# Optimization experiments

Measured on AMD Instinct MI355X. Metric: run time of the kernel, lower is better.

## Reference

```python
import jax, jax.numpy as jnp
import numpy as np

Q = 16293   # quantization_channels
R = 24      # residual_channels
D = 32      # dilation_channels
S = 128     # skip_channels
K = 2       # filter_width
NL = 8      # number of residual blocks
B = 4       # batch_size
L = 2048    # input sequence length
RECEPTIVE = (K - 1) * sum([1, 2, 4, 8, 16, 32, 64, 128]) + K  # 257
OUT_W = L - RECEPTIVE + 1  # 1792


def setup_inputs() -> dict:
    key = jax.random.key(0)
    ks = jax.random.split(key, 9)
    sc = 0.05
    return {
        "idx": jax.random.randint(ks[0], (B, L), 0, Q, dtype=jnp.int32),
        "pre_W": jax.random.normal(ks[1], (K, Q, R), jnp.float32) * sc,
        "filt_W": jax.random.normal(ks[2], (NL, K, R, D), jnp.float32) * sc,
        "gate_W": jax.random.normal(ks[3], (NL, K, R, D), jnp.float32) * sc,
        "res_W": jax.random.normal(ks[4], (NL, D, R), jnp.float32) * sc,
        "skip_W": jax.random.normal(ks[5], (NL, D, S), jnp.float32) * sc,
        "post_W1": jax.random.normal(ks[6], (S, S), jnp.float32) * sc,
        "post_W2": jax.random.normal(ks[7], (S, Q), jnp.float32) * sc,
    }


def _conv2(x, W):
    # kernel_size=2, dilation=1 (the original passes dilations[0]=1 to every
    # block), 'valid' padding: out[t] = x[t] @ W[0] + x[t+1] @ W[1]
    return jnp.einsum('btc,cf->btf', x[:, :-1], W[0]) + \
           jnp.einsum('btc,cf->btf', x[:, 1:], W[1])


def reference(idx, pre_W, filt_W, gate_W, res_W, skip_W, post_W1, post_W2):
    # one_hot(idx, Q) followed by a width-2 conv == two-tap embedding gather
    x = pre_W[0][idx[:, :-1]] + pre_W[1][idx[:, 1:]]  # [B, L-1, R]
    skip_sum = jnp.zeros((B, OUT_W, S), x.dtype)
    for i in range(NL):
        out = jnp.tanh(_conv2(x, filt_W[i])) * jax.nn.sigmoid(_conv2(x, gate_W[i]))
        # training-mode slice: skip_cut = T_out - output_width
        out_skip = out[:, -OUT_W:]                                  # [B, OUT_W, D]
        skip_sum = skip_sum + jnp.einsum('btd,ds->bts', out_skip, skip_W[i])
        transformed = jnp.einsum('btd,dr->btr', out, res_W[i])      # [B, T-1, R]
        x = x[:, 1:] + transformed                                  # residual, cut input
    h = jax.nn.relu(skip_sum)
    h = jax.nn.relu(jnp.einsum('bts,su->btu', h, post_W1))
    logits = jnp.einsum('bts,sq->btq', h, post_W2)                  # [B, OUT_W, Q]
    return logits
```

## Files before the change

### kernel.cpp

```cpp
#include <hip/hip_runtime.h>
#include <stdint.h>

#define BB 4
#define LL 2048
#define QQ 16293
#define RR 24
#define DD 32
#define SS 128
#define NLAYER 8
#define OUTW 1792
#define TT0 2047
#define MROWS (BB*OUTW)
#define NPAD 16384
#define WCH 28

typedef float v4f __attribute__((ext_vector_type(4)));
typedef short v8s __attribute__((ext_vector_type(8)));

static __device__ __forceinline__ unsigned short f2bf(float x) {
  unsigned int u = __float_as_uint(x);
  unsigned int r = (u + 0x7fffu + ((u >> 16) & 1u)) >> 16;
  return (unsigned short)r;
}

static __device__ __forceinline__ float fast_sigmoid(float z) {
  return __builtin_amdgcn_rcpf(1.0f + __expf(-z));
}
static __device__ __forceinline__ float fast_tanh(float z) {
  return 1.0f - 2.0f * __builtin_amdgcn_rcpf(1.0f + __expf(2.0f * z));
}

__global__ __launch_bounds__(1024) void fused_layers_kernel(
    const int* __restrict__ idx, const float* __restrict__ preW,
    const float* __restrict__ filtW, const float* __restrict__ gateW,
    const float* __restrict__ resW, const float* __restrict__ skipW,
    float* __restrict__ skip_out) {
  int b = blockIdx.y;
  int j0 = blockIdx.x * WCH;
  int lane = (int)(threadIdx.x & 63);
  int w = __builtin_amdgcn_readfirstlane((int)(threadIdx.x >> 6));

  __shared__ float x_t[2][RR][66];
  __shared__ float out_s[64][33];

  for (int z = (int)threadIdx.x; z < 2 * RR * 2; z += 1024) {
    int bu = z & 1;
    int cc = 64 + ((z >> 1) & 1);
    int r = z >> 2;
    x_t[bu][r][cc] = 0.f;
  }

  int tbase = j0 + 247;
  if (w < 12) {
    int t = tbase + lane;
    if (t > TT0 - 1) t = TT0 - 1;
    int i0 = idx[b * LL + t];
    int i1 = idx[b * LL + t + 1];
    const float* p0 = preW + (size_t)i0 * RR + 2 * w;
    const float* p1 = preW + (size_t)QQ * RR + (size_t)i1 * RR + 2 * w;
#pragma unroll
    for (int rr = 0; rr < 2; ++rr)
      x_t[0][2 * w + rr][lane] = p0[rr] + p1[rr];
  }

  float sk[8];
#pragma unroll
  for (int c = 0; c < 8; ++c) sk[c] = 0.f;

  __syncthreads();

  for (int i = 0; i < NLAYER; ++i) {
    int cur = i & 1, nxt = cur ^ 1;
    int lmax = 62 - i;

    float xa[RR], xb[RR];
#pragma unroll
    for (int r = 0; r < RR; ++r) {
      xa[r] = x_t[cur][r][lane];
      xb[r] = x_t[cur][r][lane + 1];
    }
    const float* Fw = filtW + (size_t)i * 2 * RR * DD;
    const float* Gw = gateW + (size_t)i * 2 * RR * DD;
    float zf[2], zg[2];
#pragma unroll
    for (int dd = 0; dd < 2; ++dd) { zf[dd] = 0.f; zg[dd] = 0.f; }
#pragma unroll
    for (int r = 0; r < RR; ++r) {
#pragma unroll
      for (int dd = 0; dd < 2; ++dd) {
        int d = w * 2 + dd;
        zf[dd] = fmaf(xa[r], Fw[r * DD + d], zf[dd]);
        zf[dd] = fmaf(xb[r], Fw[RR * DD + r * DD + d], zf[dd]);
        zg[dd] = fmaf(xa[r], Gw[r * DD + d], zg[dd]);
        zg[dd] = fmaf(xb[r], Gw[RR * DD + r * DD + d], zg[dd]);
      }
    }
    if (lane <= lmax) {
#pragma unroll
      for (int dd = 0; dd < 2; ++dd)
        out_s[lane][w * 2 + dd] = fast_tanh(zf[dd]) * fast_sigmoid(zg[dd]);
    }
    __syncthreads();

    if (lane < WCH) {
      const float* Sw = skipW + (size_t)i * DD * SS + w * 8;
#pragma unroll
      for (int d = 0; d < DD; ++d) {
        float o = out_s[lane + 7 - i][d];
#pragma unroll
        for (int c = 0; c < 8; ++c)
          sk[c] = fmaf(o, Sw[d * SS + c], sk[c]);
      }
    }

    if (w < 12 && lane <= lmax) {
      const float* Rw = resW + (size_t)i * DD * RR;
#pragma unroll
      for (int rr = 0; rr < 2; ++rr) {
        int r = w * 2 + rr;
        float acc = x_t[cur][r][lane + 1];
#pragma unroll
        for (int d = 0; d < DD; ++d)
          acc = fmaf(out_s[lane][d], Rw[d * RR + r], acc);
        x_t[nxt][r][lane] = acc;
      }
    }
    __syncthreads();
  }

  if (lane < WCH) {
    float* sp = skip_out + ((size_t)b * OUTW + j0 + lane) * SS + w * 8;
#pragma unroll
    for (int c4 = 0; c4 < 2; ++c4) {
      float4 v;
      v.x = sk[4 * c4 + 0]; v.y = sk[4 * c4 + 1];
      v.z = sk[4 * c4 + 2]; v.w = sk[4 * c4 + 3];
      *(float4*)(sp + 4 * c4) = v;
    }
  }
}

__global__ __launch_bounds__(256) void h1_kernel(const float* __restrict__ skip_sum,
                                                 const float* __restrict__ W1,
                                                 unsigned short* __restrict__ h1) {
  int m0 = blockIdx.x * 32;
  int tc = threadIdx.x & 31;
  int tr = threadIdx.x >> 5;
  __shared__ float h_s[32][128];
#pragma unroll
  for (int it = 0; it < 16; ++it) {
    int lin = it * 256 + (int)threadIdx.x;
    int rrow = lin >> 7, d = lin & 127;
    float v = skip_sum[(size_t)(m0 + rrow) * SS + d];
    h_s[rrow][d] = v > 0.f ? v : 0.f;
  }
  __syncthreads();

  float acc[4][4];
#pragma unroll
  for (int rr = 0; rr < 4; ++rr)
#pragma unroll
    for (int c = 0; c < 4; ++c) acc[rr][c] = 0.f;

#pragma unroll 4
  for (int d = 0; d < 128; ++d) {
    float4 wv = *(const float4*)(W1 + (size_t)d * SS + tc * 4);
#pragma unroll
    for (int rr = 0; rr < 4; ++rr) {
      float hv = h_s[tr * 4 + rr][d];
      acc[rr][0] = fmaf(hv, wv.x, acc[rr][0]);
      acc[rr][1] = fmaf(hv, wv.y, acc[rr][1]);
      acc[rr][2] = fmaf(hv, wv.z, acc[rr][2]);
      acc[rr][3] = fmaf(hv, wv.w, acc[rr][3]);
    }
  }
#pragma unroll
  for (int rr = 0; rr < 4; ++rr) {
    int row = m0 + tr * 4 + rr;
    ushort4 u;
    u.x = f2bf(fmaxf(acc[rr][0], 0.f));
    u.y = f2bf(fmaxf(acc[rr][1], 0.f));
    u.z = f2bf(fmaxf(acc[rr][2], 0.f));
    u.w = f2bf(fmaxf(acc[rr][3], 0.f));
    *(ushort4*)(h1 + (size_t)row * SS + tc * 4) = u;
  }
}

__global__ __launch_bounds__(256) void w2t_kernel(const float* __restrict__ W2,
                                                  unsigned short* __restrict__ W2T) {
  int n0 = blockIdx.x * 64;
  __shared__ float t_s[64][129];
#pragma unroll
  for (int it = 0; it < 32; ++it) {
    int lin = it * 256 + (int)threadIdx.x;
    int k = lin >> 6, nn = lin & 63;
    int n = n0 + nn;
    t_s[nn][k] = (n < QQ) ? W2[(size_t)k * QQ + n] : 0.f;
  }
  __syncthreads();
#pragma unroll
  for (int it = 0; it < 4; ++it) {
    int lin = it * 256 + (int)threadIdx.x;
    int nn = lin >> 4, slot = lin & 15;
    v8s val;
#pragma unroll
    for (int jj = 0; jj < 8; ++jj) val[jj] = (short)f2bf(t_s[nn][slot * 8 + jj]);
    *(v8s*)(W2T + ((size_t)(n0 + nn)) * 128 + slot * 8) = val;
  }
}

struct GemmLds {
  union {
    struct { unsigned short A_s[128 * 128]; unsigned short B_s[128 * 128]; } ab;
    float c_s[128][132];
  };
};

__global__ __launch_bounds__(256) void gemm_kernel(const unsigned short* __restrict__ A,
                                                   const unsigned short* __restrict__ Bm,
                                                   float* __restrict__ Cc) {
  __shared__ GemmLds sh;
  unsigned short* A_s = sh.ab.A_s;
  unsigned short* B_s = sh.ab.B_s;
  int m0 = blockIdx.y * 128;
  int n0 = blockIdx.x * 128;
  int tid = threadIdx.x;

#pragma unroll
  for (int it = 0; it < 8; ++it) {
    int lin = it * 256 + tid;
    int row = lin >> 4, slot = lin & 15;
    int sw = slot ^ (row & 7);
    uint4 va = *(const uint4*)(A + ((size_t)(m0 + row)) * 128 + slot * 8);
    *(uint4*)(A_s + row * 128 + sw * 8) = va;
    uint4 vb = *(const uint4*)(Bm + ((size_t)(n0 + row)) * 128 + slot * 8);
    *(uint4*)(B_s + row * 128 + sw * 8) = vb;
  }
  __syncthreads();

  int lane = tid & 63;
  int w = tid >> 6;
  int wm = (w >> 1) * 64, wn = (w & 1) * 64;
  int lr = lane & 15, g = lane >> 4;

  v4f acc[4][4];
#pragma unroll
  for (int mf = 0; mf < 4; ++mf)
#pragma unroll
    for (int nf = 0; nf < 4; ++nf) {
      v4f z = {0.f, 0.f, 0.f, 0.f};
      acc[mf][nf] = z;
    }

#pragma unroll
  for (int ks = 0; ks < 4; ++ks) {
    int kg = ks * 4 + g;
    v8s a[4], bfr[4];
#pragma unroll
    for (int mf = 0; mf < 4; ++mf) {
      int row = wm + mf * 16 + lr;
      a[mf] = *(v8s*)(A_s + row * 128 + ((kg ^ (row & 7)) * 8));
    }
#pragma unroll
    for (int nf = 0; nf < 4; ++nf) {
      int row = wn + nf * 16 + lr;
      bfr[nf] = *(v8s*)(B_s + row * 128 + ((kg ^ (row & 7)) * 8));
    }
#pragma unroll
    for (int mf = 0; mf < 4; ++mf)
#pragma unroll
      for (int nf = 0; nf < 4; ++nf)
        acc[mf][nf] = __builtin_amdgcn_mfma_f32_16x16x32_bf16(a[mf], bfr[nf], acc[mf][nf], 0, 0, 0);
  }

  __syncthreads();
#pragma unroll
  for (int mf = 0; mf < 4; ++mf)
#pragma unroll
    for (int reg = 0; reg < 4; ++reg) {
      int row = wm + mf * 16 + g * 4 + reg;
#pragma unroll
      for (int nf = 0; nf < 4; ++nf)
        sh.c_s[row][wn + nf * 16 + lr] = acc[mf][nf][reg];
    }
  __syncthreads();

  bool edge = (n0 + 128 > QQ);
  int col = tid & 127;
  int r0 = tid >> 7;
  int n = n0 + col;
  if (!edge) {
#pragma unroll
    for (int it = 0; it < 64; ++it) {
      int row = it * 2 + r0;
      Cc[(size_t)(m0 + row) * QQ + n] = sh.c_s[row][col];
    }
  } else {
    bool ok = n < QQ;
#pragma unroll
    for (int it = 0; it < 64; ++it) {
      int row = it * 2 + r0;
      if (ok) Cc[(size_t)(m0 + row) * QQ + n] = sh.c_s[row][col];
    }
  }
}

extern "C" void kernel_launch(void* const* d_in, const int* in_sizes, int n_in,
                              void* d_out, int out_size, void* d_ws, size_t ws_size,
                              hipStream_t stream) {
  (void)in_sizes; (void)n_in; (void)out_size; (void)ws_size;
  const int*   idx   = (const int*)d_in[0];
  const float* preW  = (const float*)d_in[1];
  const float* filtW = (const float*)d_in[2];
  const float* gateW = (const float*)d_in[3];
  const float* resW  = (const float*)d_in[4];
  const float* skipW = (const float*)d_in[5];
  const float* W1    = (const float*)d_in[6];
  const float* W2    = (const float*)d_in[7];
  float* out = (float*)d_out;

  char* ws = (char*)d_ws;
  float* skip = (float*)(ws);
  unsigned short* h1  = (unsigned short*)(ws + 3670016);
  unsigned short* W2T = (unsigned short*)(ws + 5505024);

  w2t_kernel<<<dim3(NPAD / 64), 256, 0, stream>>>(W2, W2T);
  fused_layers_kernel<<<dim3(OUTW / WCH, BB), 1024, 0, stream>>>(idx, preW, filtW, gateW,
                                                                 resW, skipW, skip);
  h1_kernel<<<dim3(MROWS / 32), 256, 0, stream>>>(skip, W1, h1);
  gemm_kernel<<<dim3(NPAD / 128, MROWS / 128), 256, 0, stream>>>(h1, W2T, out);
}
```

Measured before the change: 316.5 us.

## Restructure output GEMM into row-strip blocks with register-resident A and vector stores

```diff
diff --git a/kernel.cpp b/kernel.cpp
--- a/kernel.cpp
+++ b/kernel.cpp
@@ -13,6 +13,8 @@
 #define MROWS (BB*OUTW)
 #define NPAD 16384
 #define WCH 28
+#define STRIPW 2048
+#define NSTRIP 8
 
 typedef float v4f __attribute__((ext_vector_type(4)));
 typedef short v8s __attribute__((ext_vector_type(8)));
@@ -209,99 +211,103 @@
   }
 }
 
-struct GemmLds {
+struct GemmSh {
   union {
-    struct { unsigned short A_s[128 * 128]; unsigned short B_s[128 * 128]; } ab;
-    float c_s[128][132];
-  };
+    unsigned short B_s[128 * 128];
+    float c_s[32][129];
+  } u;
 };
 
 __global__ __launch_bounds__(256) void gemm_kernel(const unsigned short* __restrict__ A,
                                                    const unsigned short* __restrict__ Bm,
                                                    float* __restrict__ Cc) {
-  __shared__ GemmLds sh;
-  unsigned short* A_s = sh.ab.A_s;
-  unsigned short* B_s = sh.ab.B_s;
-  int m0 = blockIdx.y * 128;
-  int n0 = blockIdx.x * 128;
+  __shared__ GemmSh sh;
+  int strip = blockIdx.x;
+  int m0 = blockIdx.y * 32;
   int tid = threadIdx.x;
-
-#pragma unroll
-  for (int it = 0; it < 8; ++it) {
-    int lin = it * 256 + tid;
-    int row = lin >> 4, slot = lin & 15;
-    int sw = slot ^ (row & 7);
-    uint4 va = *(const uint4*)(A + ((size_t)(m0 + row)) * 128 + slot * 8);
-    *(uint4*)(A_s + row * 128 + sw * 8) = va;
-    uint4 vb = *(const uint4*)(Bm + ((size_t)(n0 + row)) * 128 + slot * 8);
-    *(uint4*)(B_s + row * 128 + sw * 8) = vb;
-  }
-  __syncthreads();
-
   int lane = tid & 63;
   int w = tid >> 6;
-  int wm = (w >> 1) * 64, wn = (w & 1) * 64;
   int lr = lane & 15, g = lane >> 4;
 
-  v4f acc[4][4];
-#pragma unroll
-  for (int mf = 0; mf < 4; ++mf)
-#pragma unroll
-    for (int nf = 0; nf < 4; ++nf) {
-      v4f z = {0.f, 0.f, 0.f, 0.f};
-      acc[mf][nf] = z;
-    }
-
-#pragma unroll
-  for (int ks = 0; ks < 4; ++ks) {
-    int kg = ks * 4 + g;
-    v8s a[4], bfr[4];
-#pragma unroll
-    for (int mf = 0; mf < 4; ++mf) {
-      int row = wm + mf * 16 + lr;
-      a[mf] = *(v8s*)(A_s + row * 128 + ((kg ^ (row & 7)) * 8));
-    }
-#pragma unroll
-    for (int nf = 0; nf < 4; ++nf) {
-      int row = wn + nf * 16 + lr;
-      bfr[nf] = *(v8s*)(B_s + row * 128 + ((kg ^ (row & 7)) * 8));
-    }
-#pragma unroll
-    for (int mf = 0; mf < 4; ++mf)
-#pragma unroll
-      for (int nf = 0; nf < 4; ++nf)
-        acc[mf][nf] = __builtin_amdgcn_mfma_f32_16x16x32_bf16(a[mf], bfr[nf], acc[mf][nf], 0, 0, 0);
-  }
-
-  __syncthreads();
-#pragma unroll
-  for (int mf = 0; mf < 4; ++mf)
-#pragma unroll
-    for (int reg = 0; reg < 4; ++reg) {
-      int row = wm + mf * 16 + g * 4 + reg;
-#pragma unroll
-      for (int nf = 0; nf < 4; ++nf)
-        sh.c_s[row][wn + nf * 16 + lr] = acc[mf][nf][reg];
-    }
-  __syncthreads();
-
-  bool edge = (n0 + 128 > QQ);
-  int col = tid & 127;
-  int r0 = tid >> 7;
-  int n = n0 + col;
-  if (!edge) {
-#pragma unroll
-    for (int it = 0; it < 64; ++it) {
-      int row = it * 2 + r0;
-      Cc[(size_t)(m0 + row) * QQ + n] = sh.c_s[row][col];
-    }
-  } else {
-    bool ok = n < QQ;
-#pragma unroll
-    for (int it = 0; it < 64; ++it) {
-      int row = it * 2 + r0;
-      if (ok) Cc[(size_t)(m0 + row) * QQ + n] = sh.c_s[row][col];
-    }
+  v8s a[2][4];
+#pragma unroll
+  for (int mf = 0; mf < 2; ++mf)
+#pragma unroll
+    for (int ks = 0; ks < 4; ++ks)
+      a[mf][ks] = *(const v8s*)(A + ((size_t)(m0 + mf * 16 + lr)) * 128 + (ks * 4 + g) * 8);
+
+  int srow = tid >> 3;
+  int sp = tid & 7;
+
+#pragma unroll 1
+  for (int c = 0; c < 16; ++c) {
+    int nb = strip * STRIPW + c * 128;
+
+#pragma unroll
+    for (int it = 0; it < 8; ++it) {
+      int lin = it * 256 + tid;
+      int row = lin >> 4, slot = lin & 15;
+      int sw = slot ^ (row & 7);
+      uint4 vb = *(const uint4*)(Bm + ((size_t)(nb + row)) * 128 + slot * 8);
+      *(uint4*)(sh.u.B_s + row * 128 + sw * 8) = vb;
+    }
+    __syncthreads();
+
+    v4f acc[2][2];
+#pragma unroll
+    for (int mf = 0; mf < 2; ++mf)
+#pragma unroll
+      for (int nf = 0; nf < 2; ++nf) {
+        v4f z = {0.f, 0.f, 0.f, 0.f};
+        acc[mf][nf] = z;
+      }
+
+#pragma unroll
+    for (int ks = 0; ks < 4; ++ks) {
+      int kg = ks * 4 + g;
+      v8s b[2];
+#pragma unroll
+      for (int nf = 0; nf < 2; ++nf) {
+        int row = w * 32 + nf * 16 + lr;
+        b[nf] = *(v8s*)(sh.u.B_s + row * 128 + ((kg ^ (row & 7)) * 8));
+      }
+#pragma unroll
+      for (int mf = 0; mf < 2; ++mf)
+#pragma unroll
+        for (int nf = 0; nf < 2; ++nf)
+          acc[mf][nf] = __builtin_amdgcn_mfma_f32_16x16x32_bf16(a[mf][ks], b[nf], acc[mf][nf], 0, 0, 0);
+    }
+    __syncthreads();
+
+#pragma unroll
+    for (int mf = 0; mf < 2; ++mf)
+#pragma unroll
+      for (int reg = 0; reg < 4; ++reg)
+#pragma unroll
+        for (int nf = 0; nf < 2; ++nf)
+          sh.u.c_s[mf * 16 + g * 4 + reg][w * 32 + nf * 16 + lr] = acc[mf][nf][reg];
+    __syncthreads();
+
+    float* crow = Cc + (size_t)(m0 + srow) * QQ;
+    if (nb + 128 <= QQ) {
+#pragma unroll
+      for (int e = 0; e < 4; ++e) {
+        int col = sp * 16 + e * 4;
+        v4f v;
+        v[0] = sh.u.c_s[srow][col + 0];
+        v[1] = sh.u.c_s[srow][col + 1];
+        v[2] = sh.u.c_s[srow][col + 2];
+        v[3] = sh.u.c_s[srow][col + 3];
+        __builtin_nontemporal_store(v, (v4f*)(crow + nb + col));
+      }
+    } else {
+#pragma unroll
+      for (int j = 0; j < 16; ++j) {
+        int n = nb + sp * 16 + j;
+        if (n < QQ) crow[n] = sh.u.c_s[srow][sp * 16 + j];
+      }
+    }
+    __syncthreads();
   }
 }
 
@@ -328,5 +334,5 @@
   fused_layers_kernel<<<dim3(OUTW / WCH, BB), 1024, 0, stream>>>(idx, preW, filtW, gateW,
                                                                  resW, skipW, skip);
   h1_kernel<<<dim3(MROWS / 32), 256, 0, stream>>>(skip, W1, h1);
-  gemm_kernel<<<dim3(NPAD / 128, MROWS / 128), 256, 0, stream>>>(h1, W2T, out);
-}
+  gemm_kernel<<<dim3(NSTRIP, MROWS / 32), 256, 0, stream>>>(h1, W2T, out);
+}
```

After: 1.010 ms. 3.19x slower.
